# Kernel optimization log

Measured on AMD Instinct MI355X. Metric: run time of the kernel, lower is better.

Reference implementation:

```python
import jax, jax.numpy as jnp
import numpy as np

D = 2048        # hidden_size
F = 1024        # moe_intermediate_size
E = 16          # num_experts
TOP_K = 2       # num_experts_per_tok
NORM_TOPK = True
B, S = 2, 1024


def setup_inputs() -> dict:
    key = jax.random.key(0)
    ks = jax.random.split(key, 6)
    scale = 0.02
    x = jax.random.normal(ks[0], (B, S, D), jnp.float32)
    w_gate = jax.random.normal(ks[1], (D, E), jnp.float32) * scale          # gate Linear (no bias)
    w_g = jax.random.normal(ks[2], (E, D, F), jnp.float32) * scale          # SwitchGLU gate_proj
    w_u = jax.random.normal(ks[3], (E, D, F), jnp.float32) * scale          # SwitchGLU up_proj
    w_d = jax.random.normal(ks[4], (E, F, D), jnp.float32) * scale          # SwitchGLU down_proj
    expert_bias = jnp.zeros((E,), jnp.float32)                              # nn.Parameter(zeros)
    return {"x": x, "w_gate": w_gate, "w_g": w_g, "w_u": w_u, "w_d": w_d,
            "expert_bias": expert_bias}


def reference(x, w_gate, w_g, w_u, w_d, expert_bias):
    xf = x.reshape(-1, D)  # [T, D] flatten tokens
    T = xf.shape[0]
    # routing: softmax in fp32, bias added AFTER softmax (as in source)
    gates = jax.nn.softmax((xf @ w_gate).astype(jnp.float32), axis=-1) + expert_bias
    scores, inds = jax.lax.top_k(gates, TOP_K)  # values gathered from biased gates
    if NORM_TOPK:
        scores = scores / (jnp.sum(scores, axis=-1, keepdims=True) + 1e-20)
    scores = scores.astype(x.dtype)
    # scatter top-k weights into dense [T, E] combine matrix (top-k inds are distinct)
    cw = jnp.zeros((T, E), x.dtype).at[jnp.arange(T)[:, None], inds].add(scores)
    # scan over experts: each step one gated-SiLU MLP + weighted accumulate
    def step(acc, inp):
        wg, wu, wd, w = inp  # wg/wu [D,F], wd [F,D], w [T]
        h = jax.nn.silu(xf @ wg) * (xf @ wu)  # [T, F]
        return acc + w[:, None] * (h @ wd), None
    y, _ = jax.lax.scan(step, jnp.zeros_like(xf), (w_g, w_u, w_d, cw.T))
    return y.reshape(x.shape)
```

## Files before the change

kernel.cpp:

```cpp
#include <hip/hip_runtime.h>
#include <hip/hip_bf16.h>

#define D_DIM 2048
#define F_DIM 1024
#define E_NUM 16
#define T_TOK 2048

typedef float f32x4 __attribute__((ext_vector_type(4)));
typedef short short8 __attribute__((ext_vector_type(8)));

__device__ inline unsigned pk2bf(float a, float b) {
    __hip_bfloat162 h2 = __float22bfloat162_rn(make_float2(a, b));
    union { __hip_bfloat162 h; unsigned u; } c; c.h = h2; return c.u;
}

__global__ __launch_bounds__(64) void k_route(const float* __restrict__ x,
                                              const float* __restrict__ wg,
                                              const float* __restrict__ bias,
                                              int* __restrict__ topk_idx,
                                              float* __restrict__ topk_w,
                                              int* __restrict__ counts) {
    int t = blockIdx.x;
    int l = threadIdx.x;
    int e = l & 15, c = l >> 4;
    const float* xr = x + (size_t)t * D_DIM + c * (D_DIM / 4);
    const float* wr = wg + (size_t)(c * (D_DIM / 4)) * E_NUM + e;
    float acc = 0.f;
#pragma unroll 4
    for (int d = 0; d < D_DIM / 4; ++d) acc += xr[d] * wr[(size_t)d * E_NUM];
    acc += __shfl_xor(acc, 16);
    acc += __shfl_xor(acc, 32);
    float m = acc;
#pragma unroll
    for (int s = 1; s < 16; s <<= 1) m = fmaxf(m, __shfl_xor(m, s));
    float p = __expf(acc - m);
    float sum = p;
#pragma unroll
    for (int s = 1; s < 16; s <<= 1) sum += __shfl_xor(sum, s);
    p = p / sum + bias[e];
    float v1 = p; int i1 = e;
#pragma unroll
    for (int s = 1; s < 16; s <<= 1) {
        float ov = __shfl_xor(v1, s); int oi = __shfl_xor(i1, s);
        if (ov > v1 || (ov == v1 && oi < i1)) { v1 = ov; i1 = oi; }
    }
    float v2 = (e == i1) ? -1e30f : p; int i2 = e;
#pragma unroll
    for (int s = 1; s < 16; s <<= 1) {
        float ov = __shfl_xor(v2, s); int oi = __shfl_xor(i2, s);
        if (ov > v2 || (ov == v2 && oi < i2)) { v2 = ov; i2 = oi; }
    }
    if (l == 0) {
        float s2 = v1 + v2 + 1e-20f;
        topk_idx[2 * t] = i1; topk_idx[2 * t + 1] = i2;
        topk_w[2 * t] = v1 / s2; topk_w[2 * t + 1] = v2 / s2;
        atomicAdd(&counts[i1], 1);
        atomicAdd(&counts[i2], 1);
    }
}

__global__ void k_offsets(const int* __restrict__ counts, int* __restrict__ offsets,
                          int* __restrict__ cursors) {
    if (threadIdx.x == 0) {
        int run = 0;
        for (int e = 0; e < E_NUM; ++e) { offsets[e] = run; cursors[e] = run; run += counts[e]; }
        offsets[E_NUM] = run;
    }
}

__global__ void k_scatter(const int* __restrict__ topk_idx, const float* __restrict__ topk_w,
                          int* __restrict__ cursors, int* __restrict__ token_ids,
                          float* __restrict__ slot_w) {
    int i = blockIdx.x * blockDim.x + threadIdx.x;
    if (i >= T_TOK * 2) return;
    int e = topk_idx[i];
    int slot = atomicAdd(&cursors[e], 1);
    token_ids[slot] = i >> 1;
    slot_w[slot] = topk_w[i];
}

__global__ __launch_bounds__(256, 3) void k_gateup(const float* __restrict__ x,
                                                   const float* __restrict__ wg_all,
                                                   const float* __restrict__ wu_all,
                                                   const int* __restrict__ offsets,
                                                   const int* __restrict__ token_ids,
                                                   __hip_bfloat16* __restrict__ hbuf) {
    int e = blockIdx.z;
    int off = offsets[e];
    int n_e = offsets[e + 1] - off;
    int m0 = blockIdx.y * 128;
    if (m0 >= n_e) return;
    int n0 = blockIdx.x * 64;
    const float* wg = wg_all + (size_t)e * (D_DIM * F_DIM);
    const float* wu = wu_all + (size_t)e * (D_DIM * F_DIM);

    __shared__ unsigned short As[2][128 * 40];
    __shared__ unsigned short Bs[2][2][64 * 40];

    int tid = threadIdx.x;
    int wid = tid >> 6, lane = tid & 63;
    int q = lane >> 4, nl = lane & 15;
    int wr = wid >> 1, wc = wid & 1;

    int arow = tid >> 1, acg = (tid & 1) * 16;
    int ag = m0 + arow;
    bool avalid = ag < n_e;
    const float* xrow = x + (size_t)(avalid ? token_ids[off + ag] : 0) * D_DIM;
    int bkr = (tid >> 4) * 2;
    int bcol = (tid & 15) * 4;

    f32x4 ra[4], rg[2], ru[2];
    f32x4 accG[4][2], accU[4][2];
#pragma unroll
    for (int ms = 0; ms < 4; ++ms)
#pragma unroll
        for (int ns = 0; ns < 2; ++ns) {
            accG[ms][ns] = (f32x4){0.f, 0.f, 0.f, 0.f};
            accU[ms][ns] = (f32x4){0.f, 0.f, 0.f, 0.f};
        }

    auto loadG = [&](int k0) {
#pragma unroll
        for (int j = 0; j < 4; ++j)
            ra[j] = avalid ? *(const f32x4*)(xrow + k0 + acg + 4 * j) : (f32x4){0.f, 0.f, 0.f, 0.f};
        size_t o0 = (size_t)(k0 + bkr) * F_DIM + n0 + bcol;
        rg[0] = *(const f32x4*)(wg + o0);
        rg[1] = *(const f32x4*)(wg + o0 + F_DIM);
        ru[0] = *(const f32x4*)(wu + o0);
        ru[1] = *(const f32x4*)(wu + o0 + F_DIM);
    };
    auto writeL = [&](int b) {
        unsigned short* a = &As[b][arow * 40 + acg];
        union { short8 v; unsigned u[4]; } w0, w1;
        w0.u[0] = pk2bf(ra[0].x, ra[0].y); w0.u[1] = pk2bf(ra[0].z, ra[0].w);
        w0.u[2] = pk2bf(ra[1].x, ra[1].y); w0.u[3] = pk2bf(ra[1].z, ra[1].w);
        w1.u[0] = pk2bf(ra[2].x, ra[2].y); w1.u[1] = pk2bf(ra[2].z, ra[2].w);
        w1.u[2] = pk2bf(ra[3].x, ra[3].y); w1.u[3] = pk2bf(ra[3].z, ra[3].w);
        *(short8*)a = w0.v; *(short8*)(a + 8) = w1.v;
#pragma unroll
        for (int j = 0; j < 4; ++j) {
            *(unsigned*)&Bs[b][0][(bcol + j) * 40 + bkr] = pk2bf(rg[0][j], rg[1][j]);
            *(unsigned*)&Bs[b][1][(bcol + j) * 40 + bkr] = pk2bf(ru[0][j], ru[1][j]);
        }
    };
    auto compute = [&](int b) {
        short8 af[4];
#pragma unroll
        for (int ms = 0; ms < 4; ++ms)
            af[ms] = *(const short8*)&As[b][(wr * 64 + ms * 16 + nl) * 40 + q * 8];
#pragma unroll
        for (int ns = 0; ns < 2; ++ns) {
            int colb = (wc * 32 + ns * 16 + nl) * 40 + q * 8;
            short8 bg = *(const short8*)&Bs[b][0][colb];
            short8 bu = *(const short8*)&Bs[b][1][colb];
#pragma unroll
            for (int ms = 0; ms < 4; ++ms) {
                accG[ms][ns] = __builtin_amdgcn_mfma_f32_16x16x32_bf16(af[ms], bg, accG[ms][ns], 0, 0, 0);
                accU[ms][ns] = __builtin_amdgcn_mfma_f32_16x16x32_bf16(af[ms], bu, accU[ms][ns], 0, 0, 0);
            }
        }
    };

    loadG(0);
    writeL(0);
    __syncthreads();
    for (int t = 0; t < D_DIM / 32; ++t) {
        int b = t & 1;
        if (t < D_DIM / 32 - 1) loadG((t + 1) * 32);
        compute(b);
        if (t < D_DIM / 32 - 1) writeL(b ^ 1);
        __syncthreads();
    }

#pragma unroll
    for (int ms = 0; ms < 4; ++ms)
#pragma unroll
        for (int j = 0; j < 4; ++j) {
            int g2 = m0 + wr * 64 + ms * 16 + q * 4 + j;
            if (g2 < n_e) {
                size_t hbase = (size_t)(off + g2) * F_DIM;
#pragma unroll
                for (int ns = 0; ns < 2; ++ns) {
                    float g = accG[ms][ns][j];
                    float u = accU[ms][ns][j];
                    float hv = (g / (1.f + __expf(-g))) * u;
                    hbuf[hbase + n0 + wc * 32 + ns * 16 + nl] = __float2bfloat16(hv);
                }
            }
        }
}

__global__ __launch_bounds__(256, 3) void k_down(const __hip_bfloat16* __restrict__ hbuf,
                                                 const float* __restrict__ wd_all,
                                                 const int* __restrict__ offsets,
                                                 const int* __restrict__ token_ids,
                                                 const float* __restrict__ slot_w,
                                                 float* __restrict__ y) {
    int e = blockIdx.z;
    int off = offsets[e];
    int n_e = offsets[e + 1] - off;
    int m0 = blockIdx.y * 128;
    if (m0 >= n_e) return;
    int n0 = blockIdx.x * 64;
    const float* wd = wd_all + (size_t)e * (F_DIM * D_DIM);

    __shared__ unsigned short As[2][128 * 40];
    __shared__ unsigned short Bs[2][64 * 40];

    int tid = threadIdx.x;
    int wid = tid >> 6, lane = tid & 63;
    int q = lane >> 4, nl = lane & 15;
    int wr = wid >> 1, wc = wid & 1;

    int arow = tid >> 1, acg = (tid & 1) * 16;
    int ag = m0 + arow;
    bool avalid = ag < n_e;
    const unsigned short* hrow = (const unsigned short*)hbuf + (size_t)(off + (avalid ? ag : 0)) * F_DIM;
    int bkr = (tid >> 4) * 2;
    int bcol = (tid & 15) * 4;

    short8 rh[2];
    f32x4 rd[2];
    f32x4 acc[4][2];
#pragma unroll
    for (int ms = 0; ms < 4; ++ms)
#pragma unroll
        for (int ns = 0; ns < 2; ++ns) acc[ms][ns] = (f32x4){0.f, 0.f, 0.f, 0.f};

    auto loadG = [&](int k0) {
        if (avalid) {
            rh[0] = *(const short8*)(hrow + k0 + acg);
            rh[1] = *(const short8*)(hrow + k0 + acg + 8);
        } else {
            rh[0] = (short8){0, 0, 0, 0, 0, 0, 0, 0};
            rh[1] = (short8){0, 0, 0, 0, 0, 0, 0, 0};
        }
        size_t o0 = (size_t)(k0 + bkr) * D_DIM + n0 + bcol;
        rd[0] = *(const f32x4*)(wd + o0);
        rd[1] = *(const f32x4*)(wd + o0 + D_DIM);
    };
    auto writeL = [&](int b) {
        unsigned short* a = &As[b][arow * 40 + acg];
        *(short8*)a = rh[0]; *(short8*)(a + 8) = rh[1];
#pragma unroll
        for (int j = 0; j < 4; ++j)
            *(unsigned*)&Bs[b][(bcol + j) * 40 + bkr] = pk2bf(rd[0][j], rd[1][j]);
    };
    auto compute = [&](int b) {
        short8 af[4];
#pragma unroll
        for (int ms = 0; ms < 4; ++ms)
            af[ms] = *(const short8*)&As[b][(wr * 64 + ms * 16 + nl) * 40 + q * 8];
#pragma unroll
        for (int ns = 0; ns < 2; ++ns) {
            short8 bd = *(const short8*)&Bs[b][(wc * 32 + ns * 16 + nl) * 40 + q * 8];
#pragma unroll
            for (int ms = 0; ms < 4; ++ms)
                acc[ms][ns] = __builtin_amdgcn_mfma_f32_16x16x32_bf16(af[ms], bd, acc[ms][ns], 0, 0, 0);
        }
    };

    loadG(0);
    writeL(0);
    __syncthreads();
    for (int t = 0; t < F_DIM / 32; ++t) {
        int b = t & 1;
        if (t < F_DIM / 32 - 1) loadG((t + 1) * 32);
        compute(b);
        if (t < F_DIM / 32 - 1) writeL(b ^ 1);
        __syncthreads();
    }

#pragma unroll
    for (int ms = 0; ms < 4; ++ms)
#pragma unroll
        for (int j = 0; j < 4; ++j) {
            int g2 = m0 + wr * 64 + ms * 16 + q * 4 + j;
            if (g2 < n_e) {
                float w = slot_w[off + g2];
                int t = token_ids[off + g2];
#pragma unroll
                for (int ns = 0; ns < 2; ++ns)
                    atomicAdd(&y[(size_t)t * D_DIM + n0 + wc * 32 + ns * 16 + nl], acc[ms][ns][j] * w);
            }
        }
}

extern "C" void kernel_launch(void* const* d_in, const int* in_sizes, int n_in,
                              void* d_out, int out_size, void* d_ws, size_t ws_size,
                              hipStream_t stream) {
    const float* x      = (const float*)d_in[0];
    const float* w_gate = (const float*)d_in[1];
    const float* w_g    = (const float*)d_in[2];
    const float* w_u    = (const float*)d_in[3];
    const float* w_d    = (const float*)d_in[4];
    const float* bias   = (const float*)d_in[5];
    float* y = (float*)d_out;

    char* ws = (char*)d_ws;
    int*   counts    = (int*)(ws + 0);
    int*   offsets   = (int*)(ws + 64);
    int*   cursors   = (int*)(ws + 192);
    int*   topk_idx  = (int*)(ws + 256);
    float* topk_w    = (float*)(ws + 256 + 16384);
    int*   token_ids = (int*)(ws + 256 + 32768);
    float* slot_w    = (float*)(ws + 256 + 49152);
    __hip_bfloat16* hbuf = (__hip_bfloat16*)(ws + 66048);

    hipMemsetAsync(ws, 0, 256, stream);
    hipMemsetAsync(d_out, 0, (size_t)out_size * sizeof(float), stream);

    k_route<<<T_TOK, 64, 0, stream>>>(x, w_gate, bias, topk_idx, topk_w, counts);
    k_offsets<<<1, 64, 0, stream>>>(counts, offsets, cursors);
    k_scatter<<<(T_TOK * 2 + 255) / 256, 256, 0, stream>>>(topk_idx, topk_w, cursors, token_ids, slot_w);
    k_gateup<<<dim3(F_DIM / 64, 16, E_NUM), 256, 0, stream>>>(x, w_g, w_u, offsets, token_ids, hbuf);
    k_down<<<dim3(D_DIM / 64, 16, E_NUM), 256, 0, stream>>>(hbuf, w_d, offsets, token_ids, slot_w, y);
}
```

Before: 339.7 us.

## Remap block order for XCD locality and vectorize transposed weight LDS stores

The 3D grid becomes a flat 1D grid. Each block index is remapped so that consecutive blocks on the same XCD (assumed round-robin across 8 XCDs) cover tiles of the same expert and N-column group, which should improve L2 reuse of weights and of x/h rows. The weight tile load also changes from float4 row loads with scattered 32-bit LDS writes to per-thread column loads of 8 k-rows. These are packed into a single 16-byte LDS store per matrix, which removes many small bank-conflicting LDS writes. In exchange, global loads become scalar 4-byte loads that are coalesced across lanes, and the k-row spacing increases the number of load instructions.

```diff
diff --git a/kernel.cpp b/kernel.cpp
--- a/kernel.cpp
+++ b/kernel.cpp
@@ -85,12 +85,16 @@
                                                    const int* __restrict__ offsets,
                                                    const int* __restrict__ token_ids,
                                                    __hip_bfloat16* __restrict__ hbuf) {
-    int e = blockIdx.z;
+    unsigned b0 = blockIdx.x;
+    unsigned w = (b0 & 7) * 512u + (b0 >> 3);
+    int e  = w >> 8;
+    int mi = w & 15;
+    int ni = (w >> 4) & 15;
     int off = offsets[e];
     int n_e = offsets[e + 1] - off;
-    int m0 = blockIdx.y * 128;
+    int m0 = mi * 128;
     if (m0 >= n_e) return;
-    int n0 = blockIdx.x * 64;
+    int n0 = ni * 64;
     const float* wg = wg_all + (size_t)e * (D_DIM * F_DIM);
     const float* wu = wu_all + (size_t)e * (D_DIM * F_DIM);
 
@@ -106,10 +110,11 @@
     int ag = m0 + arow;
     bool avalid = ag < n_e;
     const float* xrow = x + (size_t)(avalid ? token_ids[off + ag] : 0) * D_DIM;
-    int bkr = (tid >> 4) * 2;
-    int bcol = (tid & 15) * 4;
-
-    f32x4 ra[4], rg[2], ru[2];
+    int bcol = tid & 63;
+    int bkg = (tid >> 6) * 8;
+
+    f32x4 ra[4];
+    float tg[8], tu[8];
     f32x4 accG[4][2], accU[4][2];
 #pragma unroll
     for (int ms = 0; ms < 4; ++ms)
@@ -123,11 +128,13 @@
 #pragma unroll
         for (int j = 0; j < 4; ++j)
             ra[j] = avalid ? *(const f32x4*)(xrow + k0 + acg + 4 * j) : (f32x4){0.f, 0.f, 0.f, 0.f};
-        size_t o0 = (size_t)(k0 + bkr) * F_DIM + n0 + bcol;
-        rg[0] = *(const f32x4*)(wg + o0);
-        rg[1] = *(const f32x4*)(wg + o0 + F_DIM);
-        ru[0] = *(const f32x4*)(wu + o0);
-        ru[1] = *(const f32x4*)(wu + o0 + F_DIM);
+        const float* pg = wg + (size_t)(k0 + bkg) * F_DIM + n0 + bcol;
+        const float* pu = wu + (size_t)(k0 + bkg) * F_DIM + n0 + bcol;
+#pragma unroll
+        for (int i = 0; i < 8; ++i) {
+            tg[i] = pg[(size_t)i * F_DIM];
+            tu[i] = pu[(size_t)i * F_DIM];
+        }
     };
     auto writeL = [&](int b) {
         unsigned short* a = &As[b][arow * 40 + acg];
@@ -137,11 +144,14 @@
         w1.u[0] = pk2bf(ra[2].x, ra[2].y); w1.u[1] = pk2bf(ra[2].z, ra[2].w);
         w1.u[2] = pk2bf(ra[3].x, ra[3].y); w1.u[3] = pk2bf(ra[3].z, ra[3].w);
         *(short8*)a = w0.v; *(short8*)(a + 8) = w1.v;
+        union { short8 v; unsigned u[4]; } g2, u2;
 #pragma unroll
         for (int j = 0; j < 4; ++j) {
-            *(unsigned*)&Bs[b][0][(bcol + j) * 40 + bkr] = pk2bf(rg[0][j], rg[1][j]);
-            *(unsigned*)&Bs[b][1][(bcol + j) * 40 + bkr] = pk2bf(ru[0][j], ru[1][j]);
-        }
+            g2.u[j] = pk2bf(tg[2 * j], tg[2 * j + 1]);
+            u2.u[j] = pk2bf(tu[2 * j], tu[2 * j + 1]);
+        }
+        *(short8*)&Bs[b][0][bcol * 40 + bkg] = g2.v;
+        *(short8*)&Bs[b][1][bcol * 40 + bkg] = u2.v;
     };
     auto compute = [&](int b) {
         short8 af[4];
@@ -196,12 +206,16 @@
                                                  const int* __restrict__ token_ids,
                                                  const float* __restrict__ slot_w,
                                                  float* __restrict__ y) {
-    int e = blockIdx.z;
+    unsigned b0 = blockIdx.x;
+    unsigned w = (b0 & 7) * 1024u + (b0 >> 3);
+    int e  = w >> 9;
+    int mi = w & 15;
+    int ni = (w >> 4) & 31;
     int off = offsets[e];
     int n_e = offsets[e + 1] - off;
-    int m0 = blockIdx.y * 128;
+    int m0 = mi * 128;
     if (m0 >= n_e) return;
-    int n0 = blockIdx.x * 64;
+    int n0 = ni * 64;
     const float* wd = wd_all + (size_t)e * (F_DIM * D_DIM);
 
     __shared__ unsigned short As[2][128 * 40];
@@ -216,11 +230,11 @@
     int ag = m0 + arow;
     bool avalid = ag < n_e;
     const unsigned short* hrow = (const unsigned short*)hbuf + (size_t)(off + (avalid ? ag : 0)) * F_DIM;
-    int bkr = (tid >> 4) * 2;
-    int bcol = (tid & 15) * 4;
+    int bcol = tid & 63;
+    int bkg = (tid >> 6) * 8;
 
     short8 rh[2];
-    f32x4 rd[2];
+    float td[8];
     f32x4 acc[4][2];
 #pragma unroll
     for (int ms = 0; ms < 4; ++ms)
@@ -235,16 +249,17 @@
             rh[0] = (short8){0, 0, 0, 0, 0, 0, 0, 0};
             rh[1] = (short8){0, 0, 0, 0, 0, 0, 0, 0};
         }
-        size_t o0 = (size_t)(k0 + bkr) * D_DIM + n0 + bcol;
-        rd[0] = *(const f32x4*)(wd + o0);
-        rd[1] = *(const f32x4*)(wd + o0 + D_DIM);
+        const float* pd = wd + (size_t)(k0 + bkg) * D_DIM + n0 + bcol;
+#pragma unroll
+        for (int i = 0; i < 8; ++i) td[i] = pd[(size_t)i * D_DIM];
     };
     auto writeL = [&](int b) {
         unsigned short* a = &As[b][arow * 40 + acg];
         *(short8*)a = rh[0]; *(short8*)(a + 8) = rh[1];
-#pragma unroll
-        for (int j = 0; j < 4; ++j)
-            *(unsigned*)&Bs[b][(bcol + j) * 40 + bkr] = pk2bf(rd[0][j], rd[1][j]);
+        union { short8 v; unsigned u[4]; } d2;
+#pragma unroll
+        for (int j = 0; j < 4; ++j) d2.u[j] = pk2bf(td[2 * j], td[2 * j + 1]);
+        *(short8*)&Bs[b][bcol * 40 + bkg] = d2.v;
     };
     auto compute = [&](int b) {
         short8 af[4];
@@ -277,11 +292,11 @@
         for (int j = 0; j < 4; ++j) {
             int g2 = m0 + wr * 64 + ms * 16 + q * 4 + j;
             if (g2 < n_e) {
-                float w = slot_w[off + g2];
+                float w2 = slot_w[off + g2];
                 int t = token_ids[off + g2];
 #pragma unroll
                 for (int ns = 0; ns < 2; ++ns)
-                    atomicAdd(&y[(size_t)t * D_DIM + n0 + wc * 32 + ns * 16 + nl], acc[ms][ns][j] * w);
+                    atomicAdd(&y[(size_t)t * D_DIM + n0 + wc * 32 + ns * 16 + nl], acc[ms][ns][j] * w2);
             }
         }
 }
@@ -313,6 +328,6 @@
     k_route<<<T_TOK, 64, 0, stream>>>(x, w_gate, bias, topk_idx, topk_w, counts);
     k_offsets<<<1, 64, 0, stream>>>(counts, offsets, cursors);
     k_scatter<<<(T_TOK * 2 + 255) / 256, 256, 0, stream>>>(topk_idx, topk_w, cursors, token_ids, slot_w);
-    k_gateup<<<dim3(F_DIM / 64, 16, E_NUM), 256, 0, stream>>>(x, w_g, w_u, offsets, token_ids, hbuf);
-    k_down<<<dim3(D_DIM / 64, 16, E_NUM), 256, 0, stream>>>(hbuf, w_d, offsets, token_ids, slot_w, y);
-}
+    k_gateup<<<16 * 16 * E_NUM, 256, 0, stream>>>(x, w_g, w_u, offsets, token_ids, hbuf);
+    k_down<<<16 * 32 * E_NUM, 256, 0, stream>>>(hbuf, w_d, offsets, token_ids, slot_w, y);
+}
```

Result: slower. 436.9 us (+28.6%).
